# Kernel tuning notes

Measured on AMD Instinct MI355X. Metric: run time of the kernel, lower is better.

Reference implementation:

```python
import jax, jax.numpy as jnp
import numpy as np

B = 1024          # batch
X = 32 * 32       # x_neuron_num
Y = 16384         # y_neuron_num (codebook size)
Z = 1000          # z_neuron_num (classes)
P_BU = 0.5        # y_bottom_up_percent


def _l2n(a, axis):
    # F.normalize: x / max(||x||, 1e-12)
    return a / jnp.maximum(jnp.linalg.norm(a, axis=axis, keepdims=True), 1e-12)


def setup_inputs() -> dict:
    key = jax.random.key(0)
    ks = jax.random.split(key, 8)
    return {
        "x": jax.random.normal(ks[0], (B, 32, 32), jnp.float32),
        "z": jax.random.randint(ks[1], (B,), 0, Z),
        "x2y_w": jax.random.uniform(ks[2], (Y, X), jnp.float32),
        "z2y_w": jax.random.uniform(ks[3], (Y, Z), jnp.float32),
        "y2z_w": jax.random.uniform(ks[4], (Z, Y), jnp.float32),
        "y_age": jax.random.randint(ks[5], (1, Y), 0, 5).astype(jnp.float32),
        "z_age": jax.random.randint(ks[6], (1, Z), 0, 5).astype(jnp.float32),
        "y_threshold": jax.random.uniform(ks[7], (1, Y), jnp.float32) * 0.5,
        "per_item": 1,
    }


def reference(x, z, x2y_w, z2y_w, y2z_w, y_age, z_age, y_threshold, per_item):
    # one 'train' step (torch forward returns inside the per_item loop)
    batch = x.shape[0]
    x = _l2n(x.reshape(batch, -1), 1)                 # [B, X]
    z_hot = jax.nn.one_hot(z, Z, dtype=x.dtype)       # normalized one-hot == one-hot
    Wx = _l2n(x2y_w, 1)                               # [Y, X]
    Wz = _l2n(z2y_w, 1)                               # [Y, Z]
    U = _l2n(y2z_w, 1)                                # [Z, Y]

    y_pre = P_BU * (x @ Wx.T) + (1.0 - P_BU) * (z_hot @ Wz.T)  # [B, Y]

    age = y_age[0]
    thr = y_threshold[0]
    max_resp = jnp.max(y_pre, axis=1)                 # [B]
    max_idx = jnp.argmax(y_pre, axis=1)               # [B]
    # age/threshold tie-break: losers re-argmax over unactivated neurons
    judge = (max_resp > thr[max_idx]) | (age[max_idx] < 1.0)
    unact = (age < 1.0).astype(y_pre.dtype)           # [Y]
    any_unact = jnp.sum(unact) > 0
    fallback = jnp.argmax(y_pre * unact[None, :], axis=1)
    max_idx = jnp.where(judge | ~any_unact, max_idx, fallback)

    # --- Hebbian update of x2y / z2y, expressed as segment reductions ---
    # torch dense form: sum_b y_lr[b,j]*(inp[b]-W[j]) / divisor_j
    ones_b = jnp.ones((batch,), x.dtype)
    cnt = jax.ops.segment_sum(ones_b, max_idx, num_segments=Y)       # [Y]
    div = jnp.where(cnt > 0, cnt, 1.0)
    lr = 1.0 / (age + 1.0)                                           # [Y]
    sumx = jax.ops.segment_sum(x, max_idx, num_segments=Y)           # [Y, X]
    Wx_new = Wx + (lr[:, None] * (sumx - cnt[:, None] * Wx)) / div[:, None]
    sumz = jax.ops.segment_sum(z_hot, max_idx, num_segments=Y)       # [Y, Z]
    Wz_new = Wz + (lr[:, None] * (sumz - cnt[:, None] * Wz)) / div[:, None]
    age_new = age + cnt

    # --- threshold update: per-winner min response (3 for non-winners) ---
    seg_min = jax.ops.segment_min(max_resp, max_idx, num_segments=Y)
    y_cur = jnp.minimum(seg_min, 3.0)
    y_cur = jnp.where(y_cur > 2.0, 0.0, y_cur)
    y_lr_eff = jnp.where(cnt > 0, lr, 0.0)   # sum_b y_lr[b,j]/divisor_j
    thr_new = y_lr_eff * y_cur + (1.0 - y_lr_eff) * thr

    # --- y2z update, segmented by label z ---
    zage = z_age[0]
    zlr = 1.0 / (zage + 1.0)                                          # [Z]
    y_resp = jax.nn.one_hot(max_idx, Y, dtype=x.dtype)                # [B, Y]
    cz = jax.ops.segment_sum(ones_b, z, num_segments=Z)               # [Z]
    dz = jnp.where(cz > 0, cz, 1.0)
    sumy = jax.ops.segment_sum(y_resp, z, num_segments=Z)             # [Z, Y]
    U_new = U + (zlr[:, None] * (sumy - cz[:, None] * U)) / dz[:, None]
    zage_new = zage + cz

    y_activated_num = jnp.sum((age_new >= 1.0).astype(jnp.int32))
    return (y_activated_num, max_resp, Wx_new, Wz_new, U_new,
            thr_new[None, :], age_new[None, :], zage_new[None, :])
```

## Files before the change

kernel.cpp:

```cpp
#include <hip/hip_runtime.h>

#define B_N 1024
#define X_N 1024
#define Y_N 16384
#define Z_N 1000
#define KD  1024
#define MARGIN 0.004f

#define OFF_ACT      0
#define OFF_MAXRESP  1
#define OFF_WX       1025
#define OFF_WZ       16778241
#define OFF_U        33162241
#define OFF_THR      49546241
#define OFF_AGE      49562625
#define OFF_ZAGE     49579009

#define SCR_B_BYTES    4112ull
#define SCR_S_BYTES    67112976ull
#define SCR_A_BYTES    132648976ull
#define SCR_CAND_BYTES 134746128ull
#define SCR_WZT_BYTES  136843280ull

#define WS_INV_X    0
#define WS_INV_WX   1024
#define WS_INV_WZ   17408
#define WS_FIDX     38912
#define WS_CNT      39936
#define WS_ZCNT     56320
#define WS_SEGMIN   57344
#define WS_CTR      73728
#define WS_MBITS    73736
#define WS_CCNT     74248

typedef unsigned short ushort_t;
typedef _Float16 f16x8 __attribute__((ext_vector_type(8)));
typedef float f32x4 __attribute__((ext_vector_type(4)));

__device__ __forceinline__ unsigned enc_f(float f) {
    unsigned u = __float_as_uint(f);
    return (u & 0x80000000u) ? ~u : (u | 0x80000000u);
}
__device__ __forceinline__ float dec_f(unsigned e) {
    unsigned u = (e & 0x80000000u) ? (e ^ 0x80000000u) : ~e;
    return __uint_as_float(u);
}
__device__ __forceinline__ unsigned long long pack_vi(float v, int y) {
    return ((unsigned long long)enc_f(v) << 32) |
           (unsigned long long)(0xFFFFFFFFu - (unsigned)y);
}
__device__ __forceinline__ ushort_t f2h(float f) {
    _Float16 h = (_Float16)f;
    ushort_t u; __builtin_memcpy(&u, &h, 2); return u;
}
__device__ __forceinline__ float h2f(unsigned lo16) {
    ushort_t u = (ushort_t)lo16; _Float16 h;
    __builtin_memcpy(&h, &u, 2); return (float)h;
}

#define GLOAD16(gp, lp) __builtin_amdgcn_global_load_lds( \
    (const __attribute__((address_space(1))) void*)(gp),  \
    (__attribute__((address_space(3))) void*)(lp), 16, 0, 0)

__global__ void init_kernel(int* cnt, unsigned* segmin, int* zcnt, int* ctr) {
    int i = blockIdx.x * 256 + threadIdx.x;
    if (i < Y_N) { cnt[i] = 0; segmin[i] = 0xFFFFFFFFu; }
    if (i < 1024) zcnt[i] = 0;
    if (i < 8) ctr[i] = (i == 2) ? 0x7FFFFFFF : 0;
}

__global__ void unact_kernel(const float* __restrict__ y_age, int* ctr,
                             unsigned long long* __restrict__ mbits) {
    int i = blockIdx.x * 256 + threadIdx.x;
    int a = (y_age[i] < 1.0f) ? 1 : 0;
    unsigned long long m = __ballot(a);
    int mi = a ? 0x7FFFFFFF : i;
    #pragma unroll
    for (int s = 32; s > 0; s >>= 1) mi = min(mi, __shfl_xor(mi, s, 64));
    if ((threadIdx.x & 63) == 0) {
        atomicAdd(ctr, (int)__popcll(m));
        mbits[i >> 6] = m;
        if (mi != 0x7FFFFFFF) atomicMin(&ctr[2], mi);
    }
}

__global__ __launch_bounds__(256) void pack_x_kernel(
    const float* __restrict__ x, ushort_t* __restrict__ A, float* __restrict__ inv_x) {
    const int b = blockIdx.x, t = threadIdx.x;
    const int lane = t & 63, wid = t >> 6;
    float4 v = reinterpret_cast<const float4*>(x + (size_t)b * X_N)[t];
    float ss = v.x*v.x + v.y*v.y + v.z*v.z + v.w*v.w;
    #pragma unroll
    for (int s = 32; s > 0; s >>= 1) ss += __shfl_xor(ss, s, 64);
    __shared__ float red[4];
    if (lane == 0) red[wid] = ss;
    __syncthreads();
    float inv = 1.0f / fmaxf(sqrtf(red[0] + red[1] + red[2] + red[3]), 1e-12f);
    if (t == 0) inv_x[b] = inv;
    ushort_t o1[4] = { f2h(v.x*inv), f2h(v.y*inv), f2h(v.z*inv), f2h(v.w*inv) };
    *reinterpret_cast<uint2*>(A + (size_t)b * KD + t * 4) = *reinterpret_cast<uint2*>(o1);
}

__global__ __launch_bounds__(256) void pack_w_kernel(
    const float* __restrict__ wxw, const float* __restrict__ wzw,
    ushort_t* __restrict__ Bm, float* __restrict__ inv_wx, float* __restrict__ inv_wz) {
    const int y = blockIdx.x, t = threadIdx.x;
    const int lane = t & 63, wid = t >> 6;
    float4 a = reinterpret_cast<const float4*>(wxw + (size_t)y * X_N)[t];
    float4 zv = make_float4(0.f, 0.f, 0.f, 0.f);
    if (t < 250) zv = reinterpret_cast<const float4*>(wzw + (size_t)y * Z_N)[t];
    float s1 = a.x*a.x + a.y*a.y + a.z*a.z + a.w*a.w;
    float s2 = zv.x*zv.x + zv.y*zv.y + zv.z*zv.z + zv.w*zv.w;
    #pragma unroll
    for (int s = 32; s > 0; s >>= 1) {
        s1 += __shfl_xor(s1, s, 64);
        s2 += __shfl_xor(s2, s, 64);
    }
    __shared__ float r1[4], r2[4];
    if (lane == 0) { r1[wid] = s1; r2[wid] = s2; }
    __syncthreads();
    float inv1 = 1.0f / fmaxf(sqrtf(r1[0] + r1[1] + r1[2] + r1[3]), 1e-12f);
    float inv2 = 1.0f / fmaxf(sqrtf(r2[0] + r2[1] + r2[2] + r2[3]), 1e-12f);
    ushort_t o1[4] = { f2h(a.x*inv1), f2h(a.y*inv1), f2h(a.z*inv1), f2h(a.w*inv1) };
    *reinterpret_cast<uint2*>(Bm + (size_t)y * KD + t * 4) = *reinterpret_cast<uint2*>(o1);
    if (t == 0) { inv_wx[y] = inv1; inv_wz[y] = inv2; }
}

__global__ __launch_bounds__(256) void wzt_kernel(
    const float* __restrict__ wzw, const float* __restrict__ inv_wz,
    ushort_t* __restrict__ wzt) {
    const int bid = blockIdx.x;
    const int z0 = (bid & 15) * 64, y0 = (bid >> 4) * 64;
    const int t = threadIdx.x;
    __shared__ float tile[64][65];
    #pragma unroll
    for (int p = 0; p < 4; ++p) {
        int yr = p * 16 + (t >> 4);
        int z = z0 + (t & 15) * 4;
        float4 v = make_float4(0.f, 0.f, 0.f, 0.f);
        if (z + 3 < Z_N)
            v = *reinterpret_cast<const float4*>(wzw + (size_t)(y0 + yr) * Z_N + z);
        float s = 0.5f * inv_wz[y0 + yr];
        tile[(t & 15) * 4 + 0][yr] = v.x * s;
        tile[(t & 15) * 4 + 1][yr] = v.y * s;
        tile[(t & 15) * 4 + 2][yr] = v.z * s;
        tile[(t & 15) * 4 + 3][yr] = v.w * s;
    }
    __syncthreads();
    #pragma unroll
    for (int p = 0; p < 4; ++p) {
        int zr = p * 16 + (t >> 4);
        int yc = (t & 15) * 4;
        if (z0 + zr < 1024) {
            ushort_t o[4] = { f2h(tile[zr][yc]), f2h(tile[zr][yc + 1]),
                              f2h(tile[zr][yc + 2]), f2h(tile[zr][yc + 3]) };
            *reinterpret_cast<uint2*>(wzt + (size_t)(z0 + zr) * Y_N + y0 + yc) =
                *reinterpret_cast<uint2*>(o);
        }
    }
}

__global__ __launch_bounds__(512, 1) void mm256_kernel(const ushort_t* __restrict__ A,
                                                       const ushort_t* __restrict__ Bm,
                                                       ushort_t* __restrict__ S) {
    __shared__ __align__(16) _Float16 lds[4][2][1024][8];
    const int t = threadIdx.x;
    const int wid = t >> 6, lane = t & 63;
    const int bid = blockIdx.x;
    const int lb = (bid & 7) * 32 + (bid >> 3);
    const int mt = lb & 3, nt = lb >> 2;
    const int b0 = mt * 256, y0 = nt * 256;
    const int wr = wid >> 2, wc = wid & 3;
    const int r = lane & 15, gq = lane >> 4;
    const int NK = KD / 32;

    f32x4 acc[8][4];
    #pragma unroll
    for (int i = 0; i < 8; ++i)
        #pragma unroll
        for (int j = 0; j < 4; ++j) acc[i][j] = (f32x4){0.f, 0.f, 0.f, 0.f};

    auto stage = [&](int buf, int k0) {
        #pragma unroll
        for (int rr = 0; rr < 2; ++rr) {
            int s = rr * 512 + t;
            int row = s & 255, g = s >> 8;
            GLOAD16(A  + (size_t)(b0 + row) * KD + k0 + g * 8, &lds[buf][0][s][0]);
            GLOAD16(Bm + (size_t)(y0 + row) * KD + k0 + g * 8, &lds[buf][1][s][0]);
        }
    };

    stage(0, 0);
    stage(1, 32);
    stage(2, 64);
    asm volatile("s_waitcnt vmcnt(8)" ::: "memory");
    __builtin_amdgcn_s_barrier();
    asm volatile("" ::: "memory");

    for (int ks = 0; ks < NK; ++ks) {
        const int cur = ks & 3;
        f16x8 bF[4];
        #pragma unroll
        for (int nf = 0; nf < 4; ++nf)
            bF[nf] = *reinterpret_cast<const f16x8*>(
                &lds[cur][1][gq * 256 + wc * 64 + nf * 16 + r][0]);
        __builtin_amdgcn_s_setprio(1);
        #pragma unroll
        for (int mf = 0; mf < 8; ++mf) {
            f16x8 aF = *reinterpret_cast<const f16x8*>(
                &lds[cur][0][gq * 256 + wr * 128 + mf * 16 + r][0]);
            #pragma unroll
            for (int nf = 0; nf < 4; ++nf)
                acc[mf][nf] = __builtin_amdgcn_mfma_f32_16x16x32_f16(
                    aF, bF[nf], acc[mf][nf], 0, 0, 0);
        }
        __builtin_amdgcn_s_setprio(0);
        if (ks == NK - 1) break;

        __builtin_amdgcn_s_barrier();
        asm volatile("" ::: "memory");
        if (ks + 3 < NK) {
            stage((ks + 3) & 3, (ks + 3) * 32);
            asm volatile("s_waitcnt vmcnt(8)" ::: "memory");
        } else if (ks + 3 == NK) {
            asm volatile("s_waitcnt vmcnt(4)" ::: "memory");
        } else {
            asm volatile("s_waitcnt vmcnt(0)" ::: "memory");
        }
        __builtin_amdgcn_s_barrier();
        asm volatile("" ::: "memory");
    }

    #pragma unroll
    for (int mf = 0; mf < 8; ++mf) {
        int bg = b0 + wr * 128 + mf * 16 + gq * 4;
        #pragma unroll
        for (int nf = 0; nf < 4; ++nf) {
            int yg = y0 + wc * 64 + nf * 16 + r;
            f32x4 c = acc[mf][nf];
            #pragma unroll
            for (int q = 0; q < 4; ++q)
                S[(size_t)(bg + q) * Y_N + yg] = f2h(0.5f * c[q]);
        }
    }
}

__global__ __launch_bounds__(256) void scan_kernel(
    const ushort_t* __restrict__ scores, const ushort_t* __restrict__ wzt,
    const int* __restrict__ zlab, const unsigned long long* __restrict__ mbits,
    const int* __restrict__ ctr, unsigned* __restrict__ gcand, int* __restrict__ ccnt) {
    const int b = blockIdx.x, t = threadIdx.x;
    const int lane = t & 63, wid = t >> 6;
    const uint4* srow = reinterpret_cast<const uint4*>(scores + (size_t)b * Y_N);
    const uint4* wrow = reinterpret_cast<const uint4*>(wzt + (size_t)zlab[b] * Y_N);

    float vmax = -1e30f, mmax = -1e30f;
    for (int c = t; c < Y_N / 8; c += 256) {
        uint4 pk = srow[c];
        uint4 wz = wrow[c];
        int yb = c * 8;
        unsigned m8 = (unsigned)((mbits[yb >> 6] >> (yb & 63)) & 0xFFull);
        unsigned w[4] = {pk.x, pk.y, pk.z, pk.w};
        unsigned q[4] = {wz.x, wz.y, wz.z, wz.w};
        #pragma unroll
        for (int j = 0; j < 4; ++j) {
            float v0 = h2f(w[j] & 0xFFFFu) + h2f(q[j] & 0xFFFFu);
            float v1 = h2f(w[j] >> 16) + h2f(q[j] >> 16);
            vmax = fmaxf(vmax, fmaxf(v0, v1));
            mmax = fmaxf(mmax, v0 * (float)((m8 >> (2 * j)) & 1u));
            mmax = fmaxf(mmax, v1 * (float)((m8 >> (2 * j + 1)) & 1u));
        }
    }
    #pragma unroll
    for (int s = 32; s > 0; s >>= 1) {
        vmax = fmaxf(vmax, __shfl_xor(vmax, s, 64));
        mmax = fmaxf(mmax, __shfl_xor(mmax, s, 64));
    }
    __shared__ float rv[4], rm[4];
    __shared__ int nA_s, nB_s;
    __shared__ int cA[256], cB[256];
    if (lane == 0) { rv[wid] = vmax; rm[wid] = mmax; }
    if (t == 0) { nA_s = 0; nB_s = 0; }
    __syncthreads();
    float tA = fmaxf(fmaxf(rv[0], rv[1]), fmaxf(rv[2], rv[3])) - MARGIN;
    float tB = fmaxf(fmaxf(rm[0], rm[1]), fmaxf(rm[2], rm[3])) - MARGIN;
    bool anyu = ctr[0] > 0;

    for (int c = t; c < Y_N / 8; c += 256) {
        uint4 pk = srow[c];
        uint4 wz = wrow[c];
        int yb = c * 8;
        unsigned m8 = (unsigned)((mbits[yb >> 6] >> (yb & 63)) & 0xFFull);
        unsigned w[4] = {pk.x, pk.y, pk.z, pk.w};
        unsigned q[4] = {wz.x, wz.y, wz.z, wz.w};
        #pragma unroll
        for (int j = 0; j < 8; ++j) {
            unsigned sw = (j & 1) ? (w[j >> 1] >> 16) : (w[j >> 1] & 0xFFFFu);
            unsigned qw = (j & 1) ? (q[j >> 1] >> 16) : (q[j >> 1] & 0xFFFFu);
            float v = h2f(sw) + h2f(qw);
            if (v >= tA) { int p = atomicAdd(&nA_s, 1); if (p < 256) cA[p] = yb + j; }
            if (anyu && ((m8 >> j) & 1u) && v >= tB) {
                int p = atomicAdd(&nB_s, 1); if (p < 256) cB[p] = yb + j;
            }
        }
    }
    __syncthreads();
    int nA = min(nA_s, 256), nB = min(nB_s, 256);
    unsigned* slab = gcand + (size_t)b * 512;
    for (int i = t; i < nA; i += 256) slab[i] = (unsigned)cA[i];
    for (int i = t; i < nB; i += 256) slab[256 + i] = (unsigned)cB[i];
    if (t == 0) ccnt[b] = nA | (nB << 16);
}

__global__ __launch_bounds__(256) void rescore_kernel(
    const unsigned* __restrict__ gcand, const int* __restrict__ ccnt,
    const float* __restrict__ x, const float* __restrict__ inv_x,
    const float* __restrict__ wxw, const float* __restrict__ inv_wx,
    const float* __restrict__ wzw, const float* __restrict__ inv_wz,
    const int* __restrict__ zlab, const float* __restrict__ y_thr,
    const float* __restrict__ y_age, const int* __restrict__ ctr,
    int* final_idx, int* cnt, unsigned* segmin, int* zcnt,
    float* __restrict__ out_maxresp) {
    const int b = blockIdx.x, t = threadIdx.x;
    const int lane = t & 63, wid = t >> 6;
    int pc = ccnt[b];
    int nA = pc & 0xFFFF, nB = pc >> 16;
    int zb = zlab[b];
    float invx = inv_x[b];
    const unsigned* slab = gcand + (size_t)b * 512;

    const float4* xr = reinterpret_cast<const float4*>(x + (size_t)b * X_N);
    float4 xv[4];
    #pragma unroll
    for (int j = 0; j < 4; ++j) xv[j] = xr[j * 64 + lane];

    __shared__ unsigned long long red[4];
    __shared__ unsigned long long sPM;
    __shared__ int sTakeA;

    unsigned long long bA = 0ull;
    for (int c = wid; c < nA; c += 8) {
        int y1 = (int)slab[c];
        int c2 = c + 4;
        bool h2 = c2 < nA;
        int y2 = (int)slab[h2 ? c2 : c];
        const float4* w1 = reinterpret_cast<const float4*>(wxw + (size_t)y1 * X_N);
        const float4* w2 = reinterpret_cast<const float4*>(wxw + (size_t)y2 * X_N);
        float d1 = 0.f, d2 = 0.f;
        #pragma unroll
        for (int j = 0; j < 4; ++j) {
            float4 a1 = w1[j * 64 + lane];
            float4 a2 = w2[j * 64 + lane];
            d1 += xv[j].x*a1.x + xv[j].y*a1.y + xv[j].z*a1.z + xv[j].w*a1.w;
            d2 += xv[j].x*a2.x + xv[j].y*a2.y + xv[j].z*a2.z + xv[j].w*a2.w;
        }
        #pragma unroll
        for (int s = 32; s > 0; s >>= 1) {
            d1 += __shfl_xor(d1, s, 64);
            d2 += __shfl_xor(d2, s, 64);
        }
        float v1 = 0.5f*invx*inv_wx[y1]*d1 + 0.5f*inv_wz[y1]*wzw[(size_t)y1*Z_N + zb];
        unsigned long long p1 = pack_vi(v1, y1);
        bA = (p1 > bA) ? p1 : bA;
        if (h2) {
            float v2 = 0.5f*invx*inv_wx[y2]*d2 + 0.5f*inv_wz[y2]*wzw[(size_t)y2*Z_N + zb];
            unsigned long long p2 = pack_vi(v2, y2);
            bA = (p2 > bA) ? p2 : bA;
        }
    }
    if (lane == 0) red[wid] = bA;
    __syncthreads();
    if (t == 0) {
        unsigned long long pm = red[0];
        #pragma unroll
        for (int j = 1; j < 4; ++j) pm = (red[j] > pm) ? red[j] : pm;
        sPM = pm;
        unsigned enc = (unsigned)(pm >> 32);
        int idx = (int)(0xFFFFFFFFu - (unsigned)(pm & 0xFFFFFFFFull));
        float mresp = dec_f(enc);
        out_maxresp[b] = mresp;
        bool judge = (mresp > y_thr[idx]) || (y_age[idx] < 1.0f);
        bool anyu = ctr[0] > 0;
        sTakeA = (judge || !anyu) ? 1 : 0;
    }
    __syncthreads();

    if (!sTakeA) {
        unsigned long long bB = 0ull;
        for (int c = wid; c < nB; c += 8) {
            int y1 = (int)slab[256 + c];
            int c2 = c + 4;
            bool h2 = c2 < nB;
            int y2 = (int)slab[256 + (h2 ? c2 : c)];
            const float4* w1 = reinterpret_cast<const float4*>(wxw + (size_t)y1 * X_N);
            const float4* w2 = reinterpret_cast<const float4*>(wxw + (size_t)y2 * X_N);
            float d1 = 0.f, d2 = 0.f;
            #pragma unroll
            for (int j = 0; j < 4; ++j) {
                float4 a1 = w1[j * 64 + lane];
                float4 a2 = w2[j * 64 + lane];
                d1 += xv[j].x*a1.x + xv[j].y*a1.y + xv[j].z*a1.z + xv[j].w*a1.w;
                d2 += xv[j].x*a2.x + xv[j].y*a2.y + xv[j].z*a2.z + xv[j].w*a2.w;
            }
            #pragma unroll
            for (int s = 32; s > 0; s >>= 1) {
                d1 += __shfl_xor(d1, s, 64);
                d2 += __shfl_xor(d2, s, 64);
            }
            float v1 = 0.5f*invx*inv_wx[y1]*d1 + 0.5f*inv_wz[y1]*wzw[(size_t)y1*Z_N + zb];
            unsigned long long p1 = pack_vi(v1, y1);
            bB = (p1 > bB) ? p1 : bB;
            if (h2) {
                float v2 = 0.5f*invx*inv_wx[y2]*d2 + 0.5f*inv_wz[y2]*wzw[(size_t)y2*Z_N + zb];
                unsigned long long p2 = pack_vi(v2, y2);
                bB = (p2 > bB) ? p2 : bB;
            }
        }
        if (lane == 0) red[wid] = bB;
    }
    __syncthreads();
    if (t == 0) {
        unsigned long long pm = sPM;
        unsigned enc = (unsigned)(pm >> 32);
        int idx = (int)(0xFFFFFFFFu - (unsigned)(pm & 0xFFFFFFFFull));
        int fin;
        if (sTakeA) {
            fin = idx;
        } else if (nB > 0) {
            unsigned long long pf = red[0];
            #pragma unroll
            for (int j = 1; j < 4; ++j) pf = (red[j] > pf) ? red[j] : pf;
            fin = (int)(0xFFFFFFFFu - (unsigned)(pf & 0xFFFFFFFFull));
        } else {
            fin = ctr[2];
        }
        final_idx[b] = fin;
        atomicAdd(&cnt[fin], 1);
        atomicMin(&segmin[fin], enc);
        atomicAdd(&zcnt[zb], 1);
    }
}

__global__ __launch_bounds__(256) void wx_out_kernel(
    const float* __restrict__ wxw, const float* __restrict__ inv_wx,
    const float* __restrict__ x, const float* __restrict__ inv_x,
    const int* __restrict__ final_idx, const int* __restrict__ cnt,
    const float* __restrict__ y_age, float* __restrict__ outw) {
    int j = blockIdx.x;
    int t = threadIdx.x;
    __shared__ int s_b[1024];
    __shared__ int s_n;
    if (t == 0) s_n = 0;
    __syncthreads();
    int c = cnt[j];
    if (c > 0) {
        for (int b = t; b < B_N; b += 256)
            if (final_idx[b] == j) { int p = atomicAdd(&s_n, 1); s_b[p] = b; }
    }
    __syncthreads();
    float inv = inv_wx[j];
    float lr = 1.0f / (y_age[j] + 1.0f);
    float fc = (float)c;
    float dv = (c > 0) ? fc : 1.0f;
    int n = s_n;
    float4 w = *reinterpret_cast<const float4*>(wxw + (size_t)j * X_N + t * 4);
    float4 wn = make_float4(w.x*inv, w.y*inv, w.z*inv, w.w*inv);
    if (c > 0) {
        float4 s = make_float4(0.f, 0.f, 0.f, 0.f);
        for (int m = 0; m < n; ++m) {
            int b = s_b[m];
            float ix = inv_x[b];
            float4 xv = *reinterpret_cast<const float4*>(x + (size_t)b * X_N + t * 4);
            s.x += xv.x * ix; s.y += xv.y * ix; s.z += xv.z * ix; s.w += xv.w * ix;
        }
        float f = lr / dv;
        wn.x += f * (s.x - fc * wn.x);
        wn.y += f * (s.y - fc * wn.y);
        wn.z += f * (s.z - fc * wn.z);
        wn.w += f * (s.w - fc * wn.w);
    }
    *reinterpret_cast<float4*>(outw + (size_t)j * X_N + t * 4) = wn;
}

__global__ __launch_bounds__(256) void wz_out_kernel(
    const float* __restrict__ wzw, const float* __restrict__ inv_wz,
    const int* __restrict__ zlab, const int* __restrict__ final_idx,
    const int* __restrict__ cnt, const float* __restrict__ y_age,
    float* __restrict__ outw) {
    int j = blockIdx.x;
    int t = threadIdx.x;
    __shared__ int s_c[1024];
    __shared__ int s_n;
    if (t == 0) s_n = 0;
    __syncthreads();
    int c = cnt[j];
    if (c > 0) {
        for (int b = t; b < B_N; b += 256)
            if (final_idx[b] == j) { int p = atomicAdd(&s_n, 1); s_c[p] = zlab[b]; }
    }
    __syncthreads();
    if (t >= 250) return;
    float inv = inv_wz[j];
    float lr = 1.0f / (y_age[j] + 1.0f);
    float fc = (float)c;
    float dv = (c > 0) ? fc : 1.0f;
    int n = s_n;
    float4 w = *reinterpret_cast<const float4*>(wzw + (size_t)j * Z_N + t * 4);
    float4 wn = make_float4(w.x*inv, w.y*inv, w.z*inv, w.w*inv);
    if (c > 0) {
        float4 s = make_float4(0.f, 0.f, 0.f, 0.f);
        for (int m = 0; m < n; ++m) {
            int d = s_c[m] - t * 4;
            if (d == 0) s.x += 1.f;
            else if (d == 1) s.y += 1.f;
            else if (d == 2) s.z += 1.f;
            else if (d == 3) s.w += 1.f;
        }
        float f = lr / dv;
        wn.x += f * (s.x - fc * wn.x);
        wn.y += f * (s.y - fc * wn.y);
        wn.z += f * (s.z - fc * wn.z);
        wn.w += f * (s.w - fc * wn.w);
    }
    *reinterpret_cast<float4*>(outw + (size_t)j * Z_N + t * 4) = wn;
}

__global__ __launch_bounds__(256) void u_out_kernel(
    const float* __restrict__ uw, const int* __restrict__ zlab,
    const int* __restrict__ final_idx, const int* __restrict__ zcnt,
    const float* __restrict__ z_age, float* __restrict__ outw) {
    int cz = blockIdx.x;
    int t = threadIdx.x;
    const int lane = t & 63, wid = t >> 6;
    __shared__ int s_w[1024];
    __shared__ int s_n;
    __shared__ float rss[4];
    if (t == 0) s_n = 0;

    const float4* rowp4 = reinterpret_cast<const float4*>(uw + (size_t)cz * Y_N);
    float4 u[16];
    float ss = 0.f;
    #pragma unroll
    for (int p = 0; p < 16; ++p) {
        u[p] = rowp4[p * 256 + t];
        ss += u[p].x*u[p].x + u[p].y*u[p].y + u[p].z*u[p].z + u[p].w*u[p].w;
    }
    #pragma unroll
    for (int s = 32; s > 0; s >>= 1) ss += __shfl_xor(ss, s, 64);
    if (lane == 0) rss[wid] = ss;
    __syncthreads();
    float inv = 1.0f / fmaxf(sqrtf(rss[0] + rss[1] + rss[2] + rss[3]), 1e-12f);

    int c = zcnt[cz];
    if (c > 0) {
        for (int b = t; b < B_N; b += 256)
            if (zlab[b] == cz) { int p = atomicAdd(&s_n, 1); s_w[p] = final_idx[b]; }
    }
    __syncthreads();
    float zlr = 1.0f / (z_age[cz] + 1.0f);
    float fc = (float)c;
    float dv = (c > 0) ? fc : 1.0f;
    float f = zlr / dv;
    int n = s_n;
    float* outp = outw + (size_t)cz * Y_N;
    #pragma unroll
    for (int p = 0; p < 16; ++p) {
        int e4 = p * 256 + t;
        float4 un = make_float4(u[p].x*inv, u[p].y*inv, u[p].z*inv, u[p].w*inv);
        if (c > 0) {
            float4 s = make_float4(0.f, 0.f, 0.f, 0.f);
            for (int m = 0; m < n; ++m) {
                int d = s_w[m] - e4 * 4;
                if (d == 0) s.x += 1.f;
                else if (d == 1) s.y += 1.f;
                else if (d == 2) s.z += 1.f;
                else if (d == 3) s.w += 1.f;
            }
            un.x += f * (s.x - fc * un.x);
            un.y += f * (s.y - fc * un.y);
            un.z += f * (s.z - fc * un.z);
            un.w += f * (s.w - fc * un.w);
        }
        *reinterpret_cast<float4*>(outp + e4 * 4) = un;
    }
}

__global__ void thr_age_kernel(const int* __restrict__ cnt, const unsigned* __restrict__ segmin,
                               const float* __restrict__ y_age, const float* __restrict__ y_thr,
                               float* __restrict__ out_thr, float* __restrict__ out_age,
                               int* ctr) {
    int j = blockIdx.x * 256 + threadIdx.x;
    int c = cnt[j];
    float age = y_age[j];
    float thr = y_thr[j];
    float tn = thr;
    if (c > 0) {
        float lr = 1.0f / (age + 1.0f);
        float smin = dec_f(segmin[j]);
        float ycur = fminf(smin, 3.0f);
        if (ycur > 2.0f) ycur = 0.0f;
        tn = lr * ycur + (1.0f - lr) * thr;
    }
    out_thr[j] = tn;
    float an = age + (float)c;
    out_age[j] = an;
    unsigned long long m = __ballot(an >= 1.0f ? 1 : 0);
    if ((threadIdx.x & 63) == 0) atomicAdd(ctr + 1, (int)__popcll(m));
}

__global__ void zage_act_kernel(const int* __restrict__ zcnt, const float* __restrict__ z_age,
                                const int* __restrict__ ctr, float* __restrict__ out_zage,
                                float* __restrict__ out_act) {
    int i = blockIdx.x * 256 + threadIdx.x;
    if (i < Z_N) out_zage[i] = z_age[i] + (float)zcnt[i];
    if (i == 0) out_act[0] = (float)ctr[1];
}

extern "C" void kernel_launch(void* const* d_in, const int* in_sizes, int n_in,
                              void* d_out, int out_size, void* d_ws, size_t ws_size,
                              hipStream_t stream) {
    const float* x     = (const float*)d_in[0];
    const int*   z     = (const int*)d_in[1];
    const float* wxw   = (const float*)d_in[2];
    const float* wzw   = (const float*)d_in[3];
    const float* uw    = (const float*)d_in[4];
    const float* y_age = (const float*)d_in[5];
    const float* z_age = (const float*)d_in[6];
    const float* y_thr = (const float*)d_in[7];
    float* out = (float*)d_out;
    float* ws  = (float*)d_ws;
    char*  ob  = (char*)d_out;

    float* inv_x  = ws + WS_INV_X;
    float* inv_wx = ws + WS_INV_WX;
    float* inv_wz = ws + WS_INV_WZ;
    int* fidx = (int*)(ws + WS_FIDX);
    int* cnt  = (int*)(ws + WS_CNT);
    int* zcnt = (int*)(ws + WS_ZCNT);
    unsigned* segmin = (unsigned*)(ws + WS_SEGMIN);
    int* ctr = (int*)(ws + WS_CTR);
    unsigned long long* mbits = (unsigned long long*)(ws + WS_MBITS);
    int* ccnt = (int*)(ws + WS_CCNT);

    ushort_t* Bb  = (ushort_t*)(ob + SCR_B_BYTES);
    ushort_t* Sc  = (ushort_t*)(ob + SCR_S_BYTES);
    ushort_t* Ab  = (ushort_t*)(ob + SCR_A_BYTES);
    unsigned* gcand = (unsigned*)(ob + SCR_CAND_BYTES);
    ushort_t* wzt = (ushort_t*)(ob + SCR_WZT_BYTES);

    init_kernel<<<64, 256, 0, stream>>>(cnt, segmin, zcnt, ctr);
    unact_kernel<<<Y_N / 256, 256, 0, stream>>>(y_age, ctr, mbits);
    pack_x_kernel<<<B_N, 256, 0, stream>>>(x, Ab, inv_x);
    pack_w_kernel<<<Y_N, 256, 0, stream>>>(wxw, wzw, Bb, inv_wx, inv_wz);
    wzt_kernel<<<16 * 256, 256, 0, stream>>>(wzw, inv_wz, wzt);
    mm256_kernel<<<(B_N / 256) * (Y_N / 256), 512, 0, stream>>>(Ab, Bb, Sc);
    scan_kernel<<<B_N, 256, 0, stream>>>(Sc, wzt, z, mbits, ctr, gcand, ccnt);
    rescore_kernel<<<B_N, 256, 0, stream>>>(gcand, ccnt, x, inv_x, wxw, inv_wx, wzw, inv_wz,
                                            z, y_thr, y_age, ctr, fidx, cnt, segmin, zcnt,
                                            out + OFF_MAXRESP);
    wx_out_kernel<<<Y_N, 256, 0, stream>>>(wxw, inv_wx, x, inv_x, fidx, cnt, y_age, out + OFF_WX);
    wz_out_kernel<<<Y_N, 256, 0, stream>>>(wzw, inv_wz, z, fidx, cnt, y_age, out + OFF_WZ);
    u_out_kernel<<<Z_N, 256, 0, stream>>>(uw, z, fidx, zcnt, z_age, out + OFF_U);
    thr_age_kernel<<<Y_N / 256, 256, 0, stream>>>(cnt, segmin, y_age, y_thr,
                                                  out + OFF_THR, out + OFF_AGE, ctr);
    zage_act_kernel<<<4, 256, 0, stream>>>(zcnt, z_age, ctr, out + OFF_ZAGE, out + OFF_ACT);
}
```

Measured before the change: 259.0 us.

## Fuse Wz normalization with transpose and cache scan values in LDS

Moves the Wz row-norm computation out of pack_w into a new wz_prep kernel. That kernel loads 64 full Wz rows into shared memory once as fp16, computes their norms, and writes the scaled transpose, so Wz is read from global memory once instead of twice. The scan kernel also keeps the combined fp16 scores in a 32KB shared buffer during the max pass, so the threshold pass no longer re-reads scores and wzt from global memory. The costs are heavy LDS use (about 130KB in wz_prep), which limits occupancy, an extra fp16 rounding of Wz before scaling, and shared atomics for the norm sums.

```diff
diff --git a/kernel.cpp b/kernel.cpp
--- a/kernel.cpp
+++ b/kernel.cpp
@@ -102,59 +102,59 @@
 }
 
 __global__ __launch_bounds__(256) void pack_w_kernel(
-    const float* __restrict__ wxw, const float* __restrict__ wzw,
-    ushort_t* __restrict__ Bm, float* __restrict__ inv_wx, float* __restrict__ inv_wz) {
+    const float* __restrict__ wxw, ushort_t* __restrict__ Bm, float* __restrict__ inv_wx) {
     const int y = blockIdx.x, t = threadIdx.x;
     const int lane = t & 63, wid = t >> 6;
     float4 a = reinterpret_cast<const float4*>(wxw + (size_t)y * X_N)[t];
-    float4 zv = make_float4(0.f, 0.f, 0.f, 0.f);
-    if (t < 250) zv = reinterpret_cast<const float4*>(wzw + (size_t)y * Z_N)[t];
     float s1 = a.x*a.x + a.y*a.y + a.z*a.z + a.w*a.w;
-    float s2 = zv.x*zv.x + zv.y*zv.y + zv.z*zv.z + zv.w*zv.w;
-    #pragma unroll
-    for (int s = 32; s > 0; s >>= 1) {
-        s1 += __shfl_xor(s1, s, 64);
-        s2 += __shfl_xor(s2, s, 64);
-    }
-    __shared__ float r1[4], r2[4];
-    if (lane == 0) { r1[wid] = s1; r2[wid] = s2; }
+    #pragma unroll
+    for (int s = 32; s > 0; s >>= 1) s1 += __shfl_xor(s1, s, 64);
+    __shared__ float r1[4];
+    if (lane == 0) r1[wid] = s1;
     __syncthreads();
     float inv1 = 1.0f / fmaxf(sqrtf(r1[0] + r1[1] + r1[2] + r1[3]), 1e-12f);
-    float inv2 = 1.0f / fmaxf(sqrtf(r2[0] + r2[1] + r2[2] + r2[3]), 1e-12f);
     ushort_t o1[4] = { f2h(a.x*inv1), f2h(a.y*inv1), f2h(a.z*inv1), f2h(a.w*inv1) };
     *reinterpret_cast<uint2*>(Bm + (size_t)y * KD + t * 4) = *reinterpret_cast<uint2*>(o1);
-    if (t == 0) { inv_wx[y] = inv1; inv_wz[y] = inv2; }
-}
-
-__global__ __launch_bounds__(256) void wzt_kernel(
-    const float* __restrict__ wzw, const float* __restrict__ inv_wz,
-    ushort_t* __restrict__ wzt) {
-    const int bid = blockIdx.x;
-    const int z0 = (bid & 15) * 64, y0 = (bid >> 4) * 64;
+    if (t == 0) inv_wx[y] = inv1;
+}
+
+__global__ __launch_bounds__(256) void wz_prep_kernel(
+    const float* __restrict__ wzw, ushort_t* __restrict__ wzt,
+    float* __restrict__ inv_wz) {
+    const int y0 = blockIdx.x * 64;
     const int t = threadIdx.x;
-    __shared__ float tile[64][65];
-    #pragma unroll
-    for (int p = 0; p < 4; ++p) {
-        int yr = p * 16 + (t >> 4);
-        int z = z0 + (t & 15) * 4;
-        float4 v = make_float4(0.f, 0.f, 0.f, 0.f);
-        if (z + 3 < Z_N)
-            v = *reinterpret_cast<const float4*>(wzw + (size_t)(y0 + yr) * Z_N + z);
-        float s = 0.5f * inv_wz[y0 + yr];
-        tile[(t & 15) * 4 + 0][yr] = v.x * s;
-        tile[(t & 15) * 4 + 1][yr] = v.y * s;
-        tile[(t & 15) * 4 + 2][yr] = v.z * s;
-        tile[(t & 15) * 4 + 3][yr] = v.w * s;
-    }
-    __syncthreads();
-    #pragma unroll
-    for (int p = 0; p < 4; ++p) {
-        int zr = p * 16 + (t >> 4);
-        int yc = (t & 15) * 4;
-        if (z0 + zr < 1024) {
-            ushort_t o[4] = { f2h(tile[zr][yc]), f2h(tile[zr][yc + 1]),
-                              f2h(tile[zr][yc + 2]), f2h(tile[zr][yc + 3]) };
-            *reinterpret_cast<uint2*>(wzt + (size_t)(z0 + zr) * Y_N + y0 + yc) =
+    __shared__ ushort_t raw[64][1028];
+    __shared__ float ssq[64];
+    __shared__ float sinv[64];
+    if (t < 64) ssq[t] = 0.f;
+    __syncthreads();
+
+    for (int idx = t; idx < 64 * 250; idx += 256) {
+        int row = idx / 250, c4 = idx % 250;
+        float4 v = *reinterpret_cast<const float4*>(wzw + (size_t)(y0 + row) * Z_N + c4 * 4);
+        ushort_t o[4] = { f2h(v.x), f2h(v.y), f2h(v.z), f2h(v.w) };
+        *reinterpret_cast<uint2*>(&raw[row][c4 * 4]) = *reinterpret_cast<uint2*>(o);
+        atomicAdd(&ssq[row], v.x*v.x + v.y*v.y + v.z*v.z + v.w*v.w);
+    }
+    __syncthreads();
+    if (t < 64) {
+        float inv = 1.0f / fmaxf(sqrtf(ssq[t]), 1e-12f);
+        inv_wz[y0 + t] = inv;
+        sinv[t] = 0.5f * inv;
+    }
+    __syncthreads();
+
+    const int yl = (t & 15) * 4;
+    float s0 = sinv[yl + 0], s1 = sinv[yl + 1], s2 = sinv[yl + 2], s3 = sinv[yl + 3];
+    #pragma unroll 4
+    for (int p = 0; p < 64; ++p) {
+        int z = p * 16 + (t >> 4);
+        if (z < Z_N) {
+            ushort_t o[4] = { f2h(h2f(raw[yl + 0][z]) * s0),
+                              f2h(h2f(raw[yl + 1][z]) * s1),
+                              f2h(h2f(raw[yl + 2][z]) * s2),
+                              f2h(h2f(raw[yl + 3][z]) * s3) };
+            *reinterpret_cast<uint2*>(wzt + (size_t)z * Y_N + y0 + yl) =
                 *reinterpret_cast<uint2*>(o);
         }
     }
@@ -254,6 +254,11 @@
     const uint4* srow = reinterpret_cast<const uint4*>(scores + (size_t)b * Y_N);
     const uint4* wrow = reinterpret_cast<const uint4*>(wzt + (size_t)zlab[b] * Y_N);
 
+    __shared__ unsigned vbuf[Y_N / 2];
+    __shared__ float rv[4], rm[4];
+    __shared__ int nA_s, nB_s;
+    __shared__ int cA[256], cB[256];
+
     float vmax = -1e30f, mmax = -1e30f;
     for (int c = t; c < Y_N / 8; c += 256) {
         uint4 pk = srow[c];
@@ -269,6 +274,7 @@
             vmax = fmaxf(vmax, fmaxf(v0, v1));
             mmax = fmaxf(mmax, v0 * (float)((m8 >> (2 * j)) & 1u));
             mmax = fmaxf(mmax, v1 * (float)((m8 >> (2 * j + 1)) & 1u));
+            vbuf[c * 4 + j] = (unsigned)f2h(v0) | ((unsigned)f2h(v1) << 16);
         }
     }
     #pragma unroll
@@ -276,9 +282,6 @@
         vmax = fmaxf(vmax, __shfl_xor(vmax, s, 64));
         mmax = fmaxf(mmax, __shfl_xor(mmax, s, 64));
     }
-    __shared__ float rv[4], rm[4];
-    __shared__ int nA_s, nB_s;
-    __shared__ int cA[256], cB[256];
     if (lane == 0) { rv[wid] = vmax; rm[wid] = mmax; }
     if (t == 0) { nA_s = 0; nB_s = 0; }
     __syncthreads();
@@ -287,20 +290,22 @@
     bool anyu = ctr[0] > 0;
 
     for (int c = t; c < Y_N / 8; c += 256) {
-        uint4 pk = srow[c];
-        uint4 wz = wrow[c];
         int yb = c * 8;
         unsigned m8 = (unsigned)((mbits[yb >> 6] >> (yb & 63)) & 0xFFull);
-        unsigned w[4] = {pk.x, pk.y, pk.z, pk.w};
-        unsigned q[4] = {wz.x, wz.y, wz.z, wz.w};
-        #pragma unroll
-        for (int j = 0; j < 8; ++j) {
-            unsigned sw = (j & 1) ? (w[j >> 1] >> 16) : (w[j >> 1] & 0xFFFFu);
-            unsigned qw = (j & 1) ? (q[j >> 1] >> 16) : (q[j >> 1] & 0xFFFFu);
-            float v = h2f(sw) + h2f(qw);
-            if (v >= tA) { int p = atomicAdd(&nA_s, 1); if (p < 256) cA[p] = yb + j; }
-            if (anyu && ((m8 >> j) & 1u) && v >= tB) {
-                int p = atomicAdd(&nB_s, 1); if (p < 256) cB[p] = yb + j;
+        #pragma unroll
+        for (int jj = 0; jj < 4; ++jj) {
+            unsigned pv = vbuf[c * 4 + jj];
+            float v0 = h2f(pv & 0xFFFFu);
+            float v1 = h2f(pv >> 16);
+            if (v0 >= tA) { int p = atomicAdd(&nA_s, 1); if (p < 256) cA[p] = yb + 2*jj; }
+            if (v1 >= tA) { int p = atomicAdd(&nA_s, 1); if (p < 256) cA[p] = yb + 2*jj + 1; }
+            if (anyu) {
+                if (((m8 >> (2*jj)) & 1u) && v0 >= tB) {
+                    int p = atomicAdd(&nB_s, 1); if (p < 256) cB[p] = yb + 2*jj;
+                }
+                if (((m8 >> (2*jj + 1)) & 1u) && v1 >= tB) {
+                    int p = atomicAdd(&nB_s, 1); if (p < 256) cB[p] = yb + 2*jj + 1;
+                }
             }
         }
     }
@@ -651,8 +656,8 @@
     init_kernel<<<64, 256, 0, stream>>>(cnt, segmin, zcnt, ctr);
     unact_kernel<<<Y_N / 256, 256, 0, stream>>>(y_age, ctr, mbits);
     pack_x_kernel<<<B_N, 256, 0, stream>>>(x, Ab, inv_x);
-    pack_w_kernel<<<Y_N, 256, 0, stream>>>(wxw, wzw, Bb, inv_wx, inv_wz);
-    wzt_kernel<<<16 * 256, 256, 0, stream>>>(wzw, inv_wz, wzt);
+    pack_w_kernel<<<Y_N, 256, 0, stream>>>(wxw, Bb, inv_wx);
+    wz_prep_kernel<<<Y_N / 64, 256, 0, stream>>>(wzw, wzt, inv_wz);
     mm256_kernel<<<(B_N / 256) * (Y_N / 256), 512, 0, stream>>>(Ab, Bb, Sc);
     scan_kernel<<<B_N, 256, 0, stream>>>(Sc, wzt, z, mbits, ctr, gcand, ccnt);
     rescore_kernel<<<B_N, 256, 0, stream>>>(gcand, ccnt, x, inv_x, wxw, inv_wx, wzw, inv_wz,
```

Result: slower. 277.6 us (+7.2%).
